# Kernel optimization log

Hardware: AMD Instinct MI355X
Metric: run time of the kernel (lower is better)

## Reference

```python
import jax, jax.numpy as jnp
import numpy as np

B, N, D, H = 2, 2048, 1024, 16
DH = D // H  # 64 per-head dim before LRPE
EPS = 1e-5


def setup_inputs() -> dict:
    key = jax.random.key(0)
    ks = jax.random.split(key, 8)
    x = jax.random.normal(ks[0], (B, N, D), dtype=jnp.float32)
    context = jax.random.normal(ks[1], (B, N, D), dtype=jnp.float32)
    Wqkvu = jax.random.normal(ks[2], (4 * D, D), dtype=jnp.float32) * 0.02
    bqkvu = jax.random.normal(ks[3], (4 * D,), dtype=jnp.float32) * 0.02
    Wout = jax.random.normal(ks[4], (D, D), dtype=jnp.float32) * 0.02
    bout = jax.random.normal(ks[5], (D,), dtype=jnp.float32) * 0.02
    # Lrpe theta: 10000**(-2/d * arange(d)) reshaped to (H, 1, DH)
    theta = (10000.0 ** (-2.0 / D * jnp.arange(D, dtype=jnp.float32))).reshape(H, 1, DH)
    ln_w = jnp.ones((D,), dtype=jnp.float32)
    ln_b = jnp.zeros((D,), dtype=jnp.float32)
    return {"x": x, "context": context, "Wqkvu": Wqkvu, "bqkvu": bqkvu,
            "Wout": Wout, "bout": bout, "theta": theta, "ln_w": ln_w, "ln_b": ln_b}


def _lrpe(t, theta, n):
    # t: [b,h,n,d]; theta: [h,1,d]; index: [1,n,1]
    idx = jnp.arange(n, dtype=t.dtype).reshape(1, n, 1)
    th = theta * idx  # [h,n,d]
    return jnp.concatenate([t * jnp.cos(th), t * jnp.sin(th)], axis=-1)  # [b,h,n,2d]


def reference(x, context, Wqkvu, bqkvu, Wout, bout, theta, ln_w, ln_b):
    b, n, d = x.shape
    qkvu = x @ Wqkvu.T + bqkvu  # [b,n,4d]
    q, k, v, u = jnp.split(qkvu, 4, axis=-1)
    tohead = lambda t: t.reshape(b, n, H, DH).transpose(0, 2, 1, 3)  # b h n d
    q, k, v = tohead(q), tohead(k), tohead(v)
    q = jax.nn.silu(q)
    k = jax.nn.silu(k)
    q = _lrpe(q, theta, n)  # [b,h,n,2*DH]
    k = _lrpe(k, theta, n)
    # left form: materialize qk then contract with v
    qk = jnp.einsum('bhmd,bhnd->bhmn', q, k)
    out = jnp.einsum('bhmn,bhne->bhme', qk, v)  # [b,h,n,DH]
    out = out.transpose(0, 2, 1, 3).reshape(b, n, d)
    # LayerNorm
    mu = jnp.mean(out, axis=-1, keepdims=True)
    var = jnp.var(out, axis=-1, keepdims=True)
    out = (out - mu) * jax.lax.rsqrt(var + EPS) * ln_w + ln_b
    out = u * out
    return out @ Wout.T + bout
```

## Files before the change

kernel.cpp:

```cpp
#include <hip/hip_runtime.h>
#include <math.h>

#define B_ 2
#define N_ 2048
#define D_ 1024
#define H_ 16
#define DH_ 64
#define ROWS (B_*N_)
#define FOURD (4*D_)
#define EPS_ 1e-5f

typedef short bf16x8 __attribute__((ext_vector_type(8)));
typedef unsigned short u16x8 __attribute__((ext_vector_type(8)));
typedef float f32x4  __attribute__((ext_vector_type(4)));

typedef const __attribute__((address_space(1))) unsigned int* gp_t;
typedef __attribute__((address_space(3))) unsigned int* lp_t;

__device__ __forceinline__ unsigned short f2bf(float f) {
    unsigned int x = __float_as_uint(f);
    unsigned int r = (x + 0x7fffu + ((x >> 16) & 1u)) >> 16;
    return (unsigned short)r;
}
__device__ __forceinline__ float bf2f(unsigned short u) {
    return __uint_as_float((unsigned int)u << 16);
}

__global__ __launch_bounds__(256)
void cast_all(const float* __restrict__ x, const float* __restrict__ w1,
              const float* __restrict__ w2, unsigned short* __restrict__ xb,
              unsigned short* __restrict__ w1b, unsigned short* __restrict__ w2b)
{
    int i = blockIdx.x * 256 + threadIdx.x;
    const float* src; unsigned short* dst; int off;
    if (i < 1048576)      { src = x;  dst = xb;  off = i; }
    else if (i < 2097152) { src = w1; dst = w1b; off = i - 1048576; }
    else                  { src = w2; dst = w2b; off = i - 2097152; }
    float4 v = ((const float4*)src)[off];
    ushort4 o;
    o.x = f2bf(v.x); o.y = f2bf(v.y); o.z = f2bf(v.z); o.w = f2bf(v.w);
    ((ushort4*)dst)[off] = o;
}

__global__ __launch_bounds__(256)
void gemm_bt_128(const unsigned short* __restrict__ A,
                 const unsigned short* __restrict__ Bw,
                 const float* __restrict__ bias, unsigned short* __restrict__ C,
                 int M, int N, int K, int siluLim)
{
    __shared__ unsigned short As[128 * 64];
    __shared__ unsigned short Bs[128 * 64];

    const int tid  = threadIdx.x;
    const int row0 = blockIdx.y * 128;
    const int col0 = blockIdx.x * 128;
    const int wave = tid >> 6;
    const int lane = tid & 63;
    const int wr   = (wave >> 1) * 64;
    const int wc   = (wave & 1) * 64;
    const int l15  = lane & 15;
    const int quad = lane >> 4;
    const int xr   = l15 & 7;

    f32x4 acc[4][4] = {};

    const int srow = tid >> 3;
    const int skk  = ((tid & 7) ^ (srow & 7)) * 8;
    const unsigned short* ag = A  + (size_t)(row0 + srow) * K + skk;
    const unsigned short* bg = Bw + (size_t)(col0 + srow) * K + skk;
    lp_t asd = (lp_t)(void*)&As[tid * 8];
    lp_t bsd = (lp_t)(void*)&Bs[tid * 8];

    for (int k0 = 0; k0 < K; k0 += 64) {
#pragma unroll
        for (int s = 0; s < 4; ++s) {
            __builtin_amdgcn_global_load_lds((gp_t)(const void*)(ag + (size_t)(32 * s) * K + k0), asd + s * 1024, 16, 0, 0);
            __builtin_amdgcn_global_load_lds((gp_t)(const void*)(bg + (size_t)(32 * s) * K + k0), bsd + s * 1024, 16, 0, 0);
        }
        __syncthreads();

#pragma unroll
        for (int ksub = 0; ksub < 2; ++ksub) {
            const int slot = ((ksub * 4 + quad) ^ xr) * 8;
            bf16x8 af[4], bfr[4];
#pragma unroll
            for (int i = 0; i < 4; ++i)
                af[i] = *(const bf16x8*)&As[(wr + i * 16 + l15) * 64 + slot];
#pragma unroll
            for (int j = 0; j < 4; ++j)
                bfr[j] = *(const bf16x8*)&Bs[(wc + j * 16 + l15) * 64 + slot];
#pragma unroll
            for (int i = 0; i < 4; ++i)
#pragma unroll
                for (int j = 0; j < 4; ++j)
                    acc[i][j] = __builtin_amdgcn_mfma_f32_16x16x32_bf16(af[i], bfr[j], acc[i][j], 0, 0, 0);
        }
        __syncthreads();
    }

#pragma unroll
    for (int i = 0; i < 4; ++i) {
        const int r0 = row0 + wr + i * 16 + quad * 4;
#pragma unroll
        for (int j = 0; j < 4; ++j) {
            const int c = col0 + wc + j * 16 + l15;
            const float bb = bias[c];
#pragma unroll
            for (int r = 0; r < 4; ++r) {
                float v = acc[i][j][r] + bb;
                if (c < siluLim) v = v / (1.f + __expf(-v));
                C[(size_t)(r0 + r) * N + c] = f2bf(v);
            }
        }
    }
}

__global__ __launch_bounds__(256)
void gemm_bt_64(const unsigned short* __restrict__ A,
                const unsigned short* __restrict__ Bw,
                const float* __restrict__ bias, float* __restrict__ C,
                int M, int N, int K)
{
    __shared__ unsigned short As[128 * 64];
    __shared__ unsigned short Bs[64 * 64];

    const int tid  = threadIdx.x;
    const int row0 = blockIdx.y * 128;
    const int col0 = blockIdx.x * 64;
    const int wave = tid >> 6;
    const int lane = tid & 63;
    const int wr   = wave * 32;
    const int l15  = lane & 15;
    const int quad = lane >> 4;
    const int xr   = l15 & 7;

    f32x4 acc[2][4] = {};

    const int srow = tid >> 3;
    const int skk  = ((tid & 7) ^ (srow & 7)) * 8;
    const unsigned short* ag = A  + (size_t)(row0 + srow) * K + skk;
    const unsigned short* bg = Bw + (size_t)(col0 + srow) * K + skk;
    lp_t asd = (lp_t)(void*)&As[tid * 8];
    lp_t bsd = (lp_t)(void*)&Bs[tid * 8];

    for (int k0 = 0; k0 < K; k0 += 64) {
#pragma unroll
        for (int s = 0; s < 4; ++s)
            __builtin_amdgcn_global_load_lds((gp_t)(const void*)(ag + (size_t)(32 * s) * K + k0), asd + s * 1024, 16, 0, 0);
#pragma unroll
        for (int s = 0; s < 2; ++s)
            __builtin_amdgcn_global_load_lds((gp_t)(const void*)(bg + (size_t)(32 * s) * K + k0), bsd + s * 1024, 16, 0, 0);
        __syncthreads();

#pragma unroll
        for (int ksub = 0; ksub < 2; ++ksub) {
            const int slot = ((ksub * 4 + quad) ^ xr) * 8;
            bf16x8 af[2], bfr[4];
#pragma unroll
            for (int i = 0; i < 2; ++i)
                af[i] = *(const bf16x8*)&As[(wr + i * 16 + l15) * 64 + slot];
#pragma unroll
            for (int j = 0; j < 4; ++j)
                bfr[j] = *(const bf16x8*)&Bs[(j * 16 + l15) * 64 + slot];
#pragma unroll
            for (int i = 0; i < 2; ++i)
#pragma unroll
                for (int j = 0; j < 4; ++j)
                    acc[i][j] = __builtin_amdgcn_mfma_f32_16x16x32_bf16(af[i], bfr[j], acc[i][j], 0, 0, 0);
        }
        __syncthreads();
    }

#pragma unroll
    for (int i = 0; i < 2; ++i) {
        const int r0 = row0 + wr + i * 16 + quad * 4;
#pragma unroll
        for (int j = 0; j < 4; ++j) {
            const int c = col0 + j * 16 + l15;
            const float bb = bias[c];
#pragma unroll
            for (int r = 0; r < 4; ++r)
                C[(size_t)(r0 + r) * N + c] = acc[i][j][r] + bb;
        }
    }
}

__global__ __launch_bounds__(256)
void kv_mfma(const unsigned short* __restrict__ qkvu, const float* __restrict__ theta,
             float* __restrict__ part)
{
    __shared__ unsigned short kl_s[128][136];
    __shared__ unsigned short v_s [64][136];

    const int bid   = blockIdx.x;
    const int chunk = bid & 15;
    const int bh    = bid >> 4;
    const int h     = bh & 15;
    const int b     = bh >> 4;
    const int tid   = threadIdx.x;
    const int lane  = tid & 63;
    const int wave  = tid >> 6;
    const int l15   = lane & 15;
    const int quad  = lane >> 4;
    const int n0    = chunk * 128;

    for (int i = tid; i < 1024; i += 256) {
        const int nn  = i >> 3;
        const int dh0 = (i & 7) * 8;
        const int n   = n0 + nn;
        const unsigned short* qrow = qkvu + (size_t)(b * N_ + n) * FOURD;
        u16x8 k8 = *(const u16x8*)(qrow + D_     + h * DH_ + dh0);
        u16x8 v8 = *(const u16x8*)(qrow + 2 * D_ + h * DH_ + dh0);
#pragma unroll
        for (int j = 0; j < 8; ++j) {
            const int dh = dh0 + j;
            const float kf = bf2f(k8[j]);
            float s, c; __sincosf(theta[h * DH_ + dh] * (float)n, &s, &c);
            kl_s[dh][nn]      = f2bf(kf * c);
            kl_s[64 + dh][nn] = f2bf(kf * s);
            v_s[dh][nn]       = v8[j];
        }
    }
    __syncthreads();

    f32x4 acc[2][4] = {};
#pragma unroll
    for (int ks = 0; ks < 4; ++ks) {
        bf16x8 a0 = *(const bf16x8*)&kl_s[wave * 32 +      l15][ks * 32 + quad * 8];
        bf16x8 a1 = *(const bf16x8*)&kl_s[wave * 32 + 16 + l15][ks * 32 + quad * 8];
#pragma unroll
        for (int j = 0; j < 4; ++j) {
            bf16x8 bfr = *(const bf16x8*)&v_s[j * 16 + l15][ks * 32 + quad * 8];
            acc[0][j] = __builtin_amdgcn_mfma_f32_16x16x32_bf16(a0, bfr, acc[0][j], 0, 0, 0);
            acc[1][j] = __builtin_amdgcn_mfma_f32_16x16x32_bf16(a1, bfr, acc[1][j], 0, 0, 0);
        }
    }

    float* pp = part + ((size_t)bh * 16 + chunk) * 8192;
#pragma unroll
    for (int i = 0; i < 2; ++i) {
        const int d0 = wave * 32 + i * 16 + quad * 4;
#pragma unroll
        for (int j = 0; j < 4; ++j) {
            const int e = j * 16 + l15;
#pragma unroll
            for (int r = 0; r < 4; ++r)
                pp[(d0 + r) * 64 + e] = acc[i][j][r];
        }
    }
}

__global__ __launch_bounds__(256)
void kv_reduce(const float* __restrict__ part, float* __restrict__ kv)
{
    const int i  = blockIdx.x * 256 + threadIdx.x;
    const int bh = i >> 13;
    const float* pp = part + ((size_t)bh * 16) * 8192 + (i & 8191);
    float s = 0.f;
#pragma unroll
    for (int c = 0; c < 16; ++c) s += pp[c * 8192];
    kv[i] = s;
}

__global__ __launch_bounds__(256)
void attn_ln_kernel(const unsigned short* __restrict__ qkvu, const float* __restrict__ kvb,
                    const float* __restrict__ theta, const float* __restrict__ ln_w,
                    const float* __restrict__ ln_b, unsigned short* __restrict__ g)
{
    __shared__ float qc_s[8][1024];
    __shared__ float qs_s[8][1024];
    __shared__ float red[4][16];
    __shared__ float mured[8], rsred[8];

    const int row0 = blockIdx.x * 8;
    const int b    = row0 >> 11;
    const int tid  = threadIdx.x;
    const int lane = tid & 63;
    const int wave = tid >> 6;

    for (int i = tid; i < 2048; i += 256) {
        const int r  = i >> 8;
        const int c0 = (i & 255) * 4;
        const int n  = (row0 + r) & (N_ - 1);
        ushort4 qv = *(const ushort4*)&qkvu[(size_t)(row0 + r) * FOURD + c0];
        float4 tv = *(const float4*)&theta[c0];
        float q[4] = {bf2f(qv.x), bf2f(qv.y), bf2f(qv.z), bf2f(qv.w)};
        float t[4] = {tv.x, tv.y, tv.z, tv.w};
        float4 cv, sv;
        float* cp = (float*)&cv; float* sp = (float*)&sv;
#pragma unroll
        for (int j = 0; j < 4; ++j) {
            float s, c; __sincosf(t[j] * (float)n, &s, &c);
            cp[j] = q[j] * c; sp[j] = q[j] * s;
        }
        *(float4*)&qc_s[r][c0] = cv;
        *(float4*)&qs_s[r][c0] = sv;
    }
    __syncthreads();

    const int c0 = tid * 4;
    const int h  = c0 >> 6;
    const int e0 = c0 & 63;
    const float* kvp = kvb + (size_t)(b * H_ + h) * 8192;

    float o[8][4] = {};
    for (int d = 0; d < 64; ++d) {
        float4 kc = *(const float4*)&kvp[d * 64 + e0];
        float4 ks = *(const float4*)&kvp[(64 + d) * 64 + e0];
#pragma unroll
        for (int r = 0; r < 8; ++r) {
            const float qc = qc_s[r][h * 64 + d];
            const float qs = qs_s[r][h * 64 + d];
            o[r][0] = fmaf(qc, kc.x, fmaf(qs, ks.x, o[r][0]));
            o[r][1] = fmaf(qc, kc.y, fmaf(qs, ks.y, o[r][1]));
            o[r][2] = fmaf(qc, kc.z, fmaf(qs, ks.z, o[r][2]));
            o[r][3] = fmaf(qc, kc.w, fmaf(qs, ks.w, o[r][3]));
        }
    }

    float sum[8], sq[8];
#pragma unroll
    for (int r = 0; r < 8; ++r) {
        sum[r] = o[r][0] + o[r][1] + o[r][2] + o[r][3];
        sq[r]  = o[r][0]*o[r][0] + o[r][1]*o[r][1] + o[r][2]*o[r][2] + o[r][3]*o[r][3];
    }
#pragma unroll
    for (int off = 32; off; off >>= 1)
#pragma unroll
        for (int r = 0; r < 8; ++r) {
            sum[r] += __shfl_down(sum[r], off, 64);
            sq[r]  += __shfl_down(sq[r],  off, 64);
        }
    if (lane == 0)
#pragma unroll
        for (int r = 0; r < 8; ++r) { red[wave][r] = sum[r]; red[wave][8 + r] = sq[r]; }
    __syncthreads();
    if (tid < 8) {
        const float s  = red[0][tid] + red[1][tid] + red[2][tid] + red[3][tid];
        const float q2 = red[0][8+tid] + red[1][8+tid] + red[2][8+tid] + red[3][8+tid];
        const float mu = s * (1.f / (float)D_);
        const float var = q2 * (1.f / (float)D_) - mu * mu;
        mured[tid] = mu;
        rsred[tid] = rsqrtf(var + EPS_);
    }
    __syncthreads();

    float4 wv = *(const float4*)&ln_w[c0];
    float4 bv = *(const float4*)&ln_b[c0];
#pragma unroll
    for (int r = 0; r < 8; ++r) {
        ushort4 uvb = *(const ushort4*)&qkvu[(size_t)(row0 + r) * FOURD + 3 * D_ + c0];
        const float mu = mured[r], rs = rsred[r];
        ushort4 ov;
        ov.x = f2bf(((o[r][0] - mu) * rs * wv.x + bv.x) * bf2f(uvb.x));
        ov.y = f2bf(((o[r][1] - mu) * rs * wv.y + bv.y) * bf2f(uvb.y));
        ov.z = f2bf(((o[r][2] - mu) * rs * wv.z + bv.z) * bf2f(uvb.z));
        ov.w = f2bf(((o[r][3] - mu) * rs * wv.w + bv.w) * bf2f(uvb.w));
        *(ushort4*)&g[(size_t)(row0 + r) * D_ + c0] = ov;
    }
}

extern "C" void kernel_launch(void* const* d_in, const int* in_sizes, int n_in,
                              void* d_out, int out_size, void* d_ws, size_t ws_size,
                              hipStream_t stream)
{
    const float* x     = (const float*)d_in[0];
    const float* Wqkvu = (const float*)d_in[2];
    const float* bqkvu = (const float*)d_in[3];
    const float* Wout  = (const float*)d_in[4];
    const float* bout  = (const float*)d_in[5];
    const float* theta = (const float*)d_in[6];
    const float* ln_w  = (const float*)d_in[7];
    const float* ln_b  = (const float*)d_in[8];
    float* out = (float*)d_out;

    char* ws = (char*)d_ws;
    unsigned short* qkvu  = (unsigned short*)ws; ws += (size_t)ROWS * FOURD * 2;
    float*          kvbuf = (float*)ws;          ws += (size_t)B_ * H_ * 8192 * 4;
    unsigned short* wqb   = (unsigned short*)ws; ws += (size_t)FOURD * D_ * 2;
    unsigned short* wob   = (unsigned short*)ws; ws += (size_t)D_ * D_ * 2;
    unsigned short* xb    = (unsigned short*)ws; ws += (size_t)ROWS * D_ * 2;
    float*          part  = (float*)ws;
    unsigned short* gb    = (unsigned short*)ws;

    dim3 blk(256);
    cast_all<<<dim3(2359296 / 256), blk, 0, stream>>>(x, Wqkvu, Wout, xb, wqb, wob);

    gemm_bt_128<<<dim3(FOURD / 128, ROWS / 128), blk, 0, stream>>>(
        xb, wqb, bqkvu, qkvu, ROWS, FOURD, D_, 2 * D_);
    kv_mfma<<<dim3(32 * 16), blk, 0, stream>>>(qkvu, theta, part);
    kv_reduce<<<dim3(32 * 8192 / 256), blk, 0, stream>>>(part, kvbuf);
    attn_ln_kernel<<<dim3(ROWS / 8), blk, 0, stream>>>(qkvu, kvbuf, theta, ln_w, ln_b, gb);
    gemm_bt_64<<<dim3(D_ / 64, ROWS / 128), blk, 0, stream>>>(
        gb, wob, bout, out, ROWS, D_, D_);
}
```

Measured before the change: 210.1 us.

## Switch GEMMs to 32x32 MFMA, precompute LRPE tables, merge KV reduction

Both GEMMs move from 16x16x32 to 32x32x16 bf16 MFMA tiles, which cuts the number of LDS fragment loads per MFMA. A bf16 cos/sin table is precomputed in the cast kernel and reused by the KV and attention kernels in place of per-element sincos. The KV kernel now runs one 512-thread block per (batch, head) and loops over all 2048 tokens, which removes the partial buffer and the separate reduce kernel. The tradeoff is only 32 blocks for the KV stage (low parallelism), an extra 8MB table write/read, and bf16 rounding of the cos/sin values.

New measurement: 235.6 us. 12.1% more time.

```diff
diff --git a/kernel.cpp b/kernel.cpp
--- a/kernel.cpp
+++ b/kernel.cpp
@@ -13,6 +13,7 @@
 typedef short bf16x8 __attribute__((ext_vector_type(8)));
 typedef unsigned short u16x8 __attribute__((ext_vector_type(8)));
 typedef float f32x4  __attribute__((ext_vector_type(4)));
+typedef float f32x16 __attribute__((ext_vector_type(16)));
 
 typedef const __attribute__((address_space(1))) unsigned int* gp_t;
 typedef __attribute__((address_space(3))) unsigned int* lp_t;
@@ -27,19 +28,39 @@
 }
 
 __global__ __launch_bounds__(256)
-void cast_all(const float* __restrict__ x, const float* __restrict__ w1,
-              const float* __restrict__ w2, unsigned short* __restrict__ xb,
-              unsigned short* __restrict__ w1b, unsigned short* __restrict__ w2b)
+void cast_table(const float* __restrict__ x, const float* __restrict__ w1,
+                const float* __restrict__ w2, const float* __restrict__ theta,
+                unsigned short* __restrict__ xb, unsigned short* __restrict__ w1b,
+                unsigned short* __restrict__ w2b, unsigned short* __restrict__ cos_t,
+                unsigned short* __restrict__ sin_t)
 {
     int i = blockIdx.x * 256 + threadIdx.x;
-    const float* src; unsigned short* dst; int off;
-    if (i < 1048576)      { src = x;  dst = xb;  off = i; }
-    else if (i < 2097152) { src = w1; dst = w1b; off = i - 1048576; }
-    else                  { src = w2; dst = w2b; off = i - 2097152; }
-    float4 v = ((const float4*)src)[off];
-    ushort4 o;
-    o.x = f2bf(v.x); o.y = f2bf(v.y); o.z = f2bf(v.z); o.w = f2bf(v.w);
-    ((ushort4*)dst)[off] = o;
+    if (i < 2359296) {
+        const float* src; unsigned short* dst; int off;
+        if (i < 1048576)      { src = x;  dst = xb;  off = i; }
+        else if (i < 2097152) { src = w1; dst = w1b; off = i - 1048576; }
+        else                  { src = w2; dst = w2b; off = i - 2097152; }
+        float4 v = ((const float4*)src)[off];
+        ushort4 o;
+        o.x = f2bf(v.x); o.y = f2bf(v.y); o.z = f2bf(v.z); o.w = f2bf(v.w);
+        ((ushort4*)dst)[off] = o;
+    } else {
+        int j  = i - 2359296;
+        int n  = j >> 8;
+        int c0 = (j & 255) * 4;
+        float4 tv = *(const float4*)&theta[c0];
+        float t[4] = {tv.x, tv.y, tv.z, tv.w};
+        ushort4 co, si;
+        unsigned short* cp = (unsigned short*)&co;
+        unsigned short* sp = (unsigned short*)&si;
+#pragma unroll
+        for (int k = 0; k < 4; ++k) {
+            float s, c; __sincosf(t[k] * (float)n, &s, &c);
+            cp[k] = f2bf(c); sp[k] = f2bf(s);
+        }
+        *(ushort4*)&cos_t[(size_t)n * D_ + c0] = co;
+        *(ushort4*)&sin_t[(size_t)n * D_ + c0] = si;
+    }
 }
 
 __global__ __launch_bounds__(256)
@@ -58,11 +79,11 @@
     const int lane = tid & 63;
     const int wr   = (wave >> 1) * 64;
     const int wc   = (wave & 1) * 64;
-    const int l15  = lane & 15;
-    const int quad = lane >> 4;
-    const int xr   = l15 & 7;
-
-    f32x4 acc[4][4] = {};
+    const int l31  = lane & 31;
+    const int half = lane >> 5;
+    const int xr   = lane & 7;
+
+    f32x16 acc[2][2] = {};
 
     const int srow = tid >> 3;
     const int skk  = ((tid & 7) ^ (srow & 7)) * 8;
@@ -80,36 +101,33 @@
         __syncthreads();
 
 #pragma unroll
-        for (int ksub = 0; ksub < 2; ++ksub) {
-            const int slot = ((ksub * 4 + quad) ^ xr) * 8;
-            bf16x8 af[4], bfr[4];
-#pragma unroll
-            for (int i = 0; i < 4; ++i)
-                af[i] = *(const bf16x8*)&As[(wr + i * 16 + l15) * 64 + slot];
-#pragma unroll
-            for (int j = 0; j < 4; ++j)
-                bfr[j] = *(const bf16x8*)&Bs[(wc + j * 16 + l15) * 64 + slot];
-#pragma unroll
-            for (int i = 0; i < 4; ++i)
-#pragma unroll
-                for (int j = 0; j < 4; ++j)
-                    acc[i][j] = __builtin_amdgcn_mfma_f32_16x16x32_bf16(af[i], bfr[j], acc[i][j], 0, 0, 0);
-        }
-        __syncthreads();
-    }
-
-#pragma unroll
-    for (int i = 0; i < 4; ++i) {
-        const int r0 = row0 + wr + i * 16 + quad * 4;
-#pragma unroll
-        for (int j = 0; j < 4; ++j) {
-            const int c = col0 + wc + j * 16 + l15;
+        for (int ks = 0; ks < 4; ++ks) {
+            const int slot = ((ks * 2 + half) ^ xr) * 8;
+            bf16x8 a0 = *(const bf16x8*)&As[(wr +      l31) * 64 + slot];
+            bf16x8 a1 = *(const bf16x8*)&As[(wr + 32 + l31) * 64 + slot];
+            bf16x8 b0 = *(const bf16x8*)&Bs[(wc +      l31) * 64 + slot];
+            bf16x8 b1 = *(const bf16x8*)&Bs[(wc + 32 + l31) * 64 + slot];
+            acc[0][0] = __builtin_amdgcn_mfma_f32_32x32x16_bf16(a0, b0, acc[0][0], 0, 0, 0);
+            acc[0][1] = __builtin_amdgcn_mfma_f32_32x32x16_bf16(a0, b1, acc[0][1], 0, 0, 0);
+            acc[1][0] = __builtin_amdgcn_mfma_f32_32x32x16_bf16(a1, b0, acc[1][0], 0, 0, 0);
+            acc[1][1] = __builtin_amdgcn_mfma_f32_32x32x16_bf16(a1, b1, acc[1][1], 0, 0, 0);
+        }
+        __syncthreads();
+    }
+
+#pragma unroll
+    for (int i = 0; i < 2; ++i) {
+#pragma unroll
+        for (int j = 0; j < 2; ++j) {
+            const int c  = col0 + wc + j * 32 + l31;
+            const int rb = row0 + wr + i * 32 + 4 * half;
             const float bb = bias[c];
 #pragma unroll
-            for (int r = 0; r < 4; ++r) {
-                float v = acc[i][j][r] + bb;
+            for (int reg = 0; reg < 16; ++reg) {
+                const int r = rb + (reg & 3) + 8 * (reg >> 2);
+                float v = acc[i][j][reg] + bb;
                 if (c < siluLim) v = v / (1.f + __expf(-v));
-                C[(size_t)(r0 + r) * N + c] = f2bf(v);
+                C[(size_t)r * N + c] = f2bf(v);
             }
         }
     }
@@ -129,12 +147,13 @@
     const int col0 = blockIdx.x * 64;
     const int wave = tid >> 6;
     const int lane = tid & 63;
-    const int wr   = wave * 32;
-    const int l15  = lane & 15;
-    const int quad = lane >> 4;
-    const int xr   = l15 & 7;
-
-    f32x4 acc[2][4] = {};
+    const int wr   = (wave >> 1) * 64;
+    const int wc   = (wave & 1) * 32;
+    const int l31  = lane & 31;
+    const int half = lane >> 5;
+    const int xr   = lane & 7;
+
+    f32x16 acc[2] = {};
 
     const int srow = tid >> 3;
     const int skk  = ((tid & 7) ^ (srow & 7)) * 8;
@@ -153,119 +172,110 @@
         __syncthreads();
 
 #pragma unroll
-        for (int ksub = 0; ksub < 2; ++ksub) {
-            const int slot = ((ksub * 4 + quad) ^ xr) * 8;
-            bf16x8 af[2], bfr[4];
-#pragma unroll
-            for (int i = 0; i < 2; ++i)
-                af[i] = *(const bf16x8*)&As[(wr + i * 16 + l15) * 64 + slot];
-#pragma unroll
-            for (int j = 0; j < 4; ++j)
-                bfr[j] = *(const bf16x8*)&Bs[(j * 16 + l15) * 64 + slot];
-#pragma unroll
-            for (int i = 0; i < 2; ++i)
-#pragma unroll
-                for (int j = 0; j < 4; ++j)
-                    acc[i][j] = __builtin_amdgcn_mfma_f32_16x16x32_bf16(af[i], bfr[j], acc[i][j], 0, 0, 0);
-        }
-        __syncthreads();
-    }
-
+        for (int ks = 0; ks < 4; ++ks) {
+            const int slot = ((ks * 2 + half) ^ xr) * 8;
+            bf16x8 a0 = *(const bf16x8*)&As[(wr +      l31) * 64 + slot];
+            bf16x8 a1 = *(const bf16x8*)&As[(wr + 32 + l31) * 64 + slot];
+            bf16x8 b0 = *(const bf16x8*)&Bs[(wc +      l31) * 64 + slot];
+            acc[0] = __builtin_amdgcn_mfma_f32_32x32x16_bf16(a0, b0, acc[0], 0, 0, 0);
+            acc[1] = __builtin_amdgcn_mfma_f32_32x32x16_bf16(a1, b0, acc[1], 0, 0, 0);
+        }
+        __syncthreads();
+    }
+
+    const int c = col0 + wc + l31;
+    const float bb = bias[c];
 #pragma unroll
     for (int i = 0; i < 2; ++i) {
-        const int r0 = row0 + wr + i * 16 + quad * 4;
-#pragma unroll
-        for (int j = 0; j < 4; ++j) {
-            const int c = col0 + j * 16 + l15;
-            const float bb = bias[c];
-#pragma unroll
-            for (int r = 0; r < 4; ++r)
-                C[(size_t)(r0 + r) * N + c] = acc[i][j][r] + bb;
-        }
-    }
-}
-
-__global__ __launch_bounds__(256)
-void kv_mfma(const unsigned short* __restrict__ qkvu, const float* __restrict__ theta,
-             float* __restrict__ part)
-{
-    __shared__ unsigned short kl_s[128][136];
-    __shared__ unsigned short v_s [64][136];
-
-    const int bid   = blockIdx.x;
-    const int chunk = bid & 15;
-    const int bh    = bid >> 4;
-    const int h     = bh & 15;
-    const int b     = bh >> 4;
-    const int tid   = threadIdx.x;
-    const int lane  = tid & 63;
-    const int wave  = tid >> 6;
-    const int l15   = lane & 15;
-    const int quad  = lane >> 4;
-    const int n0    = chunk * 128;
-
-    for (int i = tid; i < 1024; i += 256) {
-        const int nn  = i >> 3;
-        const int dh0 = (i & 7) * 8;
-        const int n   = n0 + nn;
-        const unsigned short* qrow = qkvu + (size_t)(b * N_ + n) * FOURD;
-        u16x8 k8 = *(const u16x8*)(qrow + D_     + h * DH_ + dh0);
-        u16x8 v8 = *(const u16x8*)(qrow + 2 * D_ + h * DH_ + dh0);
+        const int rb = row0 + wr + i * 32 + 4 * half;
+#pragma unroll
+        for (int reg = 0; reg < 16; ++reg) {
+            const int r = rb + (reg & 3) + 8 * (reg >> 2);
+            C[(size_t)r * N + c] = acc[i][reg] + bb;
+        }
+    }
+}
+
+__global__ __launch_bounds__(512)
+void kv_mfma(const unsigned short* __restrict__ qkvu,
+             const unsigned short* __restrict__ cos_t,
+             const unsigned short* __restrict__ sin_t,
+             float* __restrict__ kv)
+{
+    __shared__ unsigned short kl_s[128][264];
+    __shared__ unsigned short v_s [64][264];
+
+    const int bh   = blockIdx.x;
+    const int h    = bh & 15;
+    const int b    = bh >> 4;
+    const int tid  = threadIdx.x;
+    const int lane = tid & 63;
+    const int wave = tid >> 6;
+    const int l15  = lane & 15;
+    const int quad = lane >> 4;
+    const int q4   = tid >> 3;
+    const int g    = tid & 7;
+    const int nn0  = q4 * 4;
+
+    f32x4 acc[4] = {};
+
+    for (int chunk = 0; chunk < 8; ++chunk) {
+        const int n0 = chunk * 256;
+        ushort4 pc[8], ps[8], pv[8];
+#pragma unroll
+        for (int r = 0; r < 4; ++r) {
+            const int n = n0 + nn0 + r;
+            const unsigned short* qrow = qkvu + (size_t)(b * N_ + n) * FOURD;
+            u16x8 k8 = *(const u16x8*)(qrow + D_     + h * DH_ + g * 8);
+            u16x8 v8 = *(const u16x8*)(qrow + 2 * D_ + h * DH_ + g * 8);
+            u16x8 c8 = *(const u16x8*)(cos_t + (size_t)n * D_ + h * DH_ + g * 8);
+            u16x8 s8 = *(const u16x8*)(sin_t + (size_t)n * D_ + h * DH_ + g * 8);
+#pragma unroll
+            for (int j = 0; j < 8; ++j) {
+                const float kf = bf2f(k8[j]);
+                ((unsigned short*)&pc[j])[r] = f2bf(kf * bf2f(c8[j]));
+                ((unsigned short*)&ps[j])[r] = f2bf(kf * bf2f(s8[j]));
+                ((unsigned short*)&pv[j])[r] = v8[j];
+            }
+        }
 #pragma unroll
         for (int j = 0; j < 8; ++j) {
-            const int dh = dh0 + j;
-            const float kf = bf2f(k8[j]);
-            float s, c; __sincosf(theta[h * DH_ + dh] * (float)n, &s, &c);
-            kl_s[dh][nn]      = f2bf(kf * c);
-            kl_s[64 + dh][nn] = f2bf(kf * s);
-            v_s[dh][nn]       = v8[j];
-        }
-    }
-    __syncthreads();
-
-    f32x4 acc[2][4] = {};
-#pragma unroll
-    for (int ks = 0; ks < 4; ++ks) {
-        bf16x8 a0 = *(const bf16x8*)&kl_s[wave * 32 +      l15][ks * 32 + quad * 8];
-        bf16x8 a1 = *(const bf16x8*)&kl_s[wave * 32 + 16 + l15][ks * 32 + quad * 8];
-#pragma unroll
-        for (int j = 0; j < 4; ++j) {
-            bf16x8 bfr = *(const bf16x8*)&v_s[j * 16 + l15][ks * 32 + quad * 8];
-            acc[0][j] = __builtin_amdgcn_mfma_f32_16x16x32_bf16(a0, bfr, acc[0][j], 0, 0, 0);
-            acc[1][j] = __builtin_amdgcn_mfma_f32_16x16x32_bf16(a1, bfr, acc[1][j], 0, 0, 0);
-        }
-    }
-
-    float* pp = part + ((size_t)bh * 16 + chunk) * 8192;
-#pragma unroll
-    for (int i = 0; i < 2; ++i) {
-        const int d0 = wave * 32 + i * 16 + quad * 4;
-#pragma unroll
-        for (int j = 0; j < 4; ++j) {
-            const int e = j * 16 + l15;
-#pragma unroll
-            for (int r = 0; r < 4; ++r)
-                pp[(d0 + r) * 64 + e] = acc[i][j][r];
-        }
-    }
-}
-
-__global__ __launch_bounds__(256)
-void kv_reduce(const float* __restrict__ part, float* __restrict__ kv)
-{
-    const int i  = blockIdx.x * 256 + threadIdx.x;
-    const int bh = i >> 13;
-    const float* pp = part + ((size_t)bh * 16) * 8192 + (i & 8191);
-    float s = 0.f;
-#pragma unroll
-    for (int c = 0; c < 16; ++c) s += pp[c * 8192];
-    kv[i] = s;
+            const int dh = g * 8 + j;
+            *(ushort4*)&kl_s[dh][nn0]      = pc[j];
+            *(ushort4*)&kl_s[64 + dh][nn0] = ps[j];
+            *(ushort4*)&v_s[dh][nn0]       = pv[j];
+        }
+        __syncthreads();
+
+#pragma unroll
+        for (int ks = 0; ks < 8; ++ks) {
+            bf16x8 a = *(const bf16x8*)&kl_s[wave * 16 + l15][ks * 32 + quad * 8];
+#pragma unroll
+            for (int j = 0; j < 4; ++j) {
+                bf16x8 bfr = *(const bf16x8*)&v_s[j * 16 + l15][ks * 32 + quad * 8];
+                acc[j] = __builtin_amdgcn_mfma_f32_16x16x32_bf16(a, bfr, acc[j], 0, 0, 0);
+            }
+        }
+        __syncthreads();
+    }
+
+    float* kvp = kv + (size_t)bh * 8192;
+    const int d0 = wave * 16 + quad * 4;
+#pragma unroll
+    for (int j = 0; j < 4; ++j) {
+        const int e = j * 16 + l15;
+#pragma unroll
+        for (int r = 0; r < 4; ++r)
+            kvp[(d0 + r) * 64 + e] = acc[j][r];
+    }
 }
 
 __global__ __launch_bounds__(256)
 void attn_ln_kernel(const unsigned short* __restrict__ qkvu, const float* __restrict__ kvb,
-                    const float* __restrict__ theta, const float* __restrict__ ln_w,
-                    const float* __restrict__ ln_b, unsigned short* __restrict__ g)
+                    const unsigned short* __restrict__ cos_t,
+                    const unsigned short* __restrict__ sin_t,
+                    const float* __restrict__ ln_w, const float* __restrict__ ln_b,
+                    unsigned short* __restrict__ g)
 {
     __shared__ float qc_s[8][1024];
     __shared__ float qs_s[8][1024];
@@ -280,21 +290,18 @@
 
     for (int i = tid; i < 2048; i += 256) {
         const int r  = i >> 8;
-        const int c0 = (i & 255) * 4;
+        const int ci = (i & 255) * 4;
         const int n  = (row0 + r) & (N_ - 1);
-        ushort4 qv = *(const ushort4*)&qkvu[(size_t)(row0 + r) * FOURD + c0];
-        float4 tv = *(const float4*)&theta[c0];
-        float q[4] = {bf2f(qv.x), bf2f(qv.y), bf2f(qv.z), bf2f(qv.w)};
-        float t[4] = {tv.x, tv.y, tv.z, tv.w};
-        float4 cv, sv;
-        float* cp = (float*)&cv; float* sp = (float*)&sv;
-#pragma unroll
-        for (int j = 0; j < 4; ++j) {
-            float s, c; __sincosf(t[j] * (float)n, &s, &c);
-            cp[j] = q[j] * c; sp[j] = q[j] * s;
-        }
-        *(float4*)&qc_s[r][c0] = cv;
-        *(float4*)&qs_s[r][c0] = sv;
+        ushort4 qv = *(const ushort4*)&qkvu[(size_t)(row0 + r) * FOURD + ci];
+        ushort4 cv = *(const ushort4*)&cos_t[(size_t)n * D_ + ci];
+        ushort4 sv = *(const ushort4*)&sin_t[(size_t)n * D_ + ci];
+        float4 co, so;
+        co.x = bf2f(qv.x) * bf2f(cv.x); so.x = bf2f(qv.x) * bf2f(sv.x);
+        co.y = bf2f(qv.y) * bf2f(cv.y); so.y = bf2f(qv.y) * bf2f(sv.y);
+        co.z = bf2f(qv.z) * bf2f(cv.z); so.z = bf2f(qv.z) * bf2f(sv.z);
+        co.w = bf2f(qv.w) * bf2f(cv.w); so.w = bf2f(qv.w) * bf2f(sv.w);
+        *(float4*)&qc_s[r][ci] = co;
+        *(float4*)&qs_s[r][ci] = so;
     }
     __syncthreads();
 
@@ -380,17 +387,19 @@
     unsigned short* wqb   = (unsigned short*)ws; ws += (size_t)FOURD * D_ * 2;
     unsigned short* wob   = (unsigned short*)ws; ws += (size_t)D_ * D_ * 2;
     unsigned short* xb    = (unsigned short*)ws; ws += (size_t)ROWS * D_ * 2;
-    float*          part  = (float*)ws;
+    unsigned short* cost  = (unsigned short*)ws; ws += (size_t)N_ * D_ * 2;
+    unsigned short* sint  = (unsigned short*)ws; ws += (size_t)N_ * D_ * 2;
     unsigned short* gb    = (unsigned short*)ws;
 
     dim3 blk(256);
-    cast_all<<<dim3(2359296 / 256), blk, 0, stream>>>(x, Wqkvu, Wout, xb, wqb, wob);
+    cast_table<<<dim3(2883584 / 256), blk, 0, stream>>>(
+        x, Wqkvu, Wout, theta, xb, wqb, wob, cost, sint);
 
     gemm_bt_128<<<dim3(FOURD / 128, ROWS / 128), blk, 0, stream>>>(
         xb, wqb, bqkvu, qkvu, ROWS, FOURD, D_, 2 * D_);
-    kv_mfma<<<dim3(32 * 16), blk, 0, stream>>>(qkvu, theta, part);
-    kv_reduce<<<dim3(32 * 8192 / 256), blk, 0, stream>>>(part, kvbuf);
-    attn_ln_kernel<<<dim3(ROWS / 8), blk, 0, stream>>>(qkvu, kvbuf, theta, ln_w, ln_b, gb);
+    kv_mfma<<<dim3(B_ * H_), dim3(512), 0, stream>>>(qkvu, cost, sint, kvbuf);
+    attn_ln_kernel<<<dim3(ROWS / 8), blk, 0, stream>>>(
+        qkvu, kvbuf, cost, sint, ln_w, ln_b, gb);
     gemm_bt_64<<<dim3(D_ / 64, ROWS / 128), blk, 0, stream>>>(
         gb, wob, bout, out, ROWS, D_, D_);
 }
```
